# Kernel optimization log

Hardware: AMD Instinct MI355X
Metric: run time of the kernel (lower is better)

## Reference

```python
import jax, jax.numpy as jnp
import numpy as np

DIVISOR = 2.0
NEGATIVE_SLOPE = 0.01


def setup_inputs() -> dict:
    key = jax.random.key(0)
    k1, k2, k3 = jax.random.split(key, 3)
    x = jax.random.normal(k1, (32, 128, 130, 130), dtype=jnp.float32)
    weight = jax.random.normal(k2, (256, 128, 3, 3), dtype=jnp.float32) * 0.05
    bias = jax.random.normal(k3, (256,), dtype=jnp.float32)
    return {"x": x, "weight": weight, "bias": bias}


def reference(x, weight, bias):
    # conv2d, stride=1, padding=0 (VALID), NCHW / OIHW layout
    y = jax.lax.conv_general_dilated(
        x, weight,
        window_strides=(1, 1),
        padding='VALID',
        dimension_numbers=('NCHW', 'OIHW', 'NCHW'),
    )
    y = y + bias[None, :, None, None]
    y = y * (1.0 / DIVISOR)
    # fused LeakyReLU epilogue
    return jnp.where(y >= 0, y, y * NEGATIVE_SLOPE)
```

## Files before the change

kernel.cpp:

```cpp
#include <hip/hip_runtime.h>
#include <hip/hip_bf16.h>
#include <stdint.h>

typedef __bf16 bf16x8 __attribute__((ext_vector_type(8)));
typedef float  f32x4  __attribute__((ext_vector_type(4)));

#define NSLOPE 0.01f

#define NB   32
#define CIN  128
#define HIN  130
#define WIN  130
#define KOUT 256
#define POUT 128
#define QOUT 128
#define HWIN (HIN*WIN)
#define PQ   (POUT*QOUT)

#define XP_BYTES 138444800ull
#define WP_ELEMS (2*3*3*KOUT*64)

#define XT_OFF    16384
#define LDS_TOTAL (16384 + 16640)

__device__ __forceinline__ unsigned short f2bf(float f) {
    unsigned u = __builtin_bit_cast(unsigned, f);
    u += 0x7FFFu + ((u >> 16) & 1u);
    return (unsigned short)(u >> 16);
}

__device__ __forceinline__ void g2lds16(const void* g, void* l) {
    __builtin_amdgcn_global_load_lds(
        (const __attribute__((address_space(1))) void*)g,
        (__attribute__((address_space(3))) void*)l,
        16, 0, 0);
}

__global__ __launch_bounds__(256) void k_conv_xw(const float* __restrict__ X,
                                                 const float* __restrict__ W,
                                                 unsigned short* __restrict__ Xp,
                                                 unsigned short* __restrict__ Wp) {
    __shared__ unsigned int tile[64*131];
    const int tid = threadIdx.x;

    if (blockIdx.x >= NB*HIN) {
        int e = (blockIdx.x - NB*HIN)*256 + tid;
        if (e < WP_ELEMS) {
            int ci = e & 63;
            int k  = (e >> 6) & 255;
            int rsIdx = e >> 14;
            int cc = rsIdx / 9; int rem = rsIdx - cc*9; int r = rem / 3, s = rem - r*3;
            int c = cc*64 + ci;
            Wp[e] = f2bf(W[(size_t)k*1152 + (size_t)c*9 + r*3 + s]);
        }
        return;
    }

    const int b = blockIdx.x;
    const int n = b / 130, h = b - n*130;
    const size_t in0 = (size_t)n*(CIN*(size_t)HWIN) + (size_t)h*WIN;
    for (int fi = tid; fi < 64*130; fi += 256) {
        const int c2 = fi / 130, w = fi - c2*130;
        const float lo = X[in0 + (size_t)(2*c2  )*HWIN + w];
        const float hi = X[in0 + (size_t)(2*c2+1)*HWIN + w];
        tile[c2*131 + w] = (unsigned)f2bf(lo) | ((unsigned)f2bf(hi) << 16);
    }
    __syncthreads();
    unsigned int* outp = (unsigned int*)(Xp + (size_t)b*(WIN*CIN));
    for (int oi = tid; oi < 2080; oi += 256) {
        const int w = oi >> 4, j4 = (oi & 15) << 2;
        uint4 v;
        v.x = tile[(j4+0)*131 + w];
        v.y = tile[(j4+1)*131 + w];
        v.z = tile[(j4+2)*131 + w];
        v.w = tile[(j4+3)*131 + w];
        *(uint4*)(outp + w*64 + j4) = v;
    }
}

template<int PRIO>
__device__ __forceinline__ void conv_body(
    const unsigned short* __restrict__ Xp,
    const unsigned short* __restrict__ Wp,
    const float* __restrict__ bias,
    float* __restrict__ out,
    unsigned char* smem, int tid, int L)
{
    const int lane = tid & 63;
    const int wm   = tid >> 6;
    const int l15  = lane & 15;
    const int kg16 = (lane >> 4) << 4;

    const int kh = L & 1;
    const int np = L >> 1;
    const int p  = np & 127;
    const int n  = np >> 7;

    f32x4 acc[4][8];
    #pragma unroll
    for (int i = 0; i < 4; ++i)
        #pragma unroll
        for (int j = 0; j < 8; ++j)
            acc[i][j] = (f32x4){0.f, 0.f, 0.f, 0.f};

    #pragma unroll 1
    for (int t = 0; t < 18; ++t) {
        const int cc = t / 9;
        const int rem = t - cc*9;
        const int r  = rem / 3;
        const int s  = rem - r*3;

        __syncthreads();

        {
            const unsigned short* wbase = Wp + (size_t)t*(KOUT*64) + (size_t)(kh*128)*64;
            #pragma unroll
            for (int it = 0; it < 8; ++it) {
                const int g    = it*128 + tid;
                const int phys = g << 4;
                const int row  = phys >> 7;
                const int cib  = (phys & 127) ^ ((row & 7) << 4);
                g2lds16(wbase + (size_t)row*64 + (cib >> 1), smem + phys);
            }
        }
        if (s == 0) {
            const unsigned short* xbase =
                Xp + ((size_t)((n*HIN + (p + r))*WIN))*CIN + cc*64;
            #pragma unroll
            for (int it = 0; it < 9; ++it) {
                const int g = it*128 + tid;
                if (g < 1040) {
                    const int phys = g << 4;
                    const int w    = phys >> 7;
                    const int cib  = (phys & 127) ^ ((w & 7) << 4);
                    g2lds16(xbase + (size_t)w*CIN + (cib >> 1), smem + XT_OFF + phys);
                }
            }
        }

        __syncthreads();

        #pragma unroll
        for (int kq = 0; kq < 2; ++kq) {
            const int cib0 = kq*64 + kg16;
            bf16x8 A[4], B[8];
            #pragma unroll
            for (int mf = 0; mf < 4; ++mf) {
                const int row = wm*64 + mf*16 + l15;
                A[mf] = *(const bf16x8*)(smem + row*128 + (cib0 ^ ((row & 7) << 4)));
            }
            #pragma unroll
            for (int nf = 0; nf < 8; ++nf) {
                const int g = nf*16 + l15 + s;
                B[nf] = *(const bf16x8*)(smem + XT_OFF + g*128 + (cib0 ^ ((g & 7) << 4)));
            }
            __builtin_amdgcn_s_setprio(PRIO + 1);
            #pragma unroll
            for (int mf = 0; mf < 4; ++mf)
                #pragma unroll
                for (int nf = 0; nf < 8; ++nf)
                    acc[mf][nf] = __builtin_amdgcn_mfma_f32_16x16x32_bf16(
                        A[mf], B[nf], acc[mf][nf], 0, 0, 0);
            __builtin_amdgcn_s_setprio(PRIO);
        }
    }

    const int kg = lane >> 4;
    #pragma unroll
    for (int mf = 0; mf < 4; ++mf) {
        const int kb = kh*128 + wm*64 + mf*16 + kg*4;
        const float4 bv = *(const float4*)(bias + kb);
        const float bj[4] = {bv.x, bv.y, bv.z, bv.w};
        #pragma unroll
        for (int nf = 0; nf < 8; ++nf) {
            const int q = nf*16 + l15;
            const size_t base = (((size_t)n*KOUT + kb)*POUT + p)*QOUT + q;
            #pragma unroll
            for (int j = 0; j < 4; ++j) {
                float y = (acc[mf][nf][j] + bj[j]) * 0.5f;
                out[base + (size_t)j*PQ] = (y >= 0.f) ? y : y*NSLOPE;
            }
        }
    }
}

__global__ __launch_bounds__(128, 2) void k_conv_main(
    const unsigned short* __restrict__ Xp,
    const unsigned short* __restrict__ Wp,
    const float* __restrict__ bias,
    float* __restrict__ out)
{
    __shared__ __align__(16) unsigned char smem[LDS_TOTAL];

    const int L = ((blockIdx.x & 7) << 10) | (blockIdx.x >> 3);

    if (blockIdx.x & 1) {
        __builtin_amdgcn_s_setprio(1);
        conv_body<1>(Xp, Wp, bias, out, smem, threadIdx.x, L);
    } else {
        conv_body<0>(Xp, Wp, bias, out, smem, threadIdx.x, L);
    }
}

extern "C" void kernel_launch(void* const* d_in, const int* in_sizes, int n_in,
                              void* d_out, int out_size, void* d_ws, size_t ws_size,
                              hipStream_t stream) {
    const float* X = (const float*)d_in[0];
    const float* W = (const float*)d_in[1];
    const float* B = (const float*)d_in[2];
    float* out = (float*)d_out;
    unsigned short* Xp = (unsigned short*)d_ws;
    unsigned short* Wp = (unsigned short*)((char*)d_ws + XP_BYTES);

    k_conv_xw  <<<NB*HIN + (WP_ELEMS + 255)/256, 256, 0, stream>>>(X, W, Xp, Wp);
    k_conv_main<<<8192, 128, 0, stream>>>(Xp, Wp, B, out);
}
```

Baseline: 391.3 us.

## Double-buffer weight tiles in LDS and prefetch next tap during MFMA

Weight tiles are now double-buffered in LDS. The next tap's weight slice is issued with global_load_lds before the current tap's MFMAs run. Explicit vmcnt waits and raw s_barrier calls with sched_barrier fences replace the two __syncthreads per iteration. The input row tile stays single-buffered and is loaded at the start of each filter row. LDS use per block grows by 16KB, which could limit occupancy, and the hand-placed waitcnts depend on the order in which loads are issued.

```diff
diff --git a/kernel.cpp b/kernel.cpp
--- a/kernel.cpp
+++ b/kernel.cpp
@@ -20,8 +20,12 @@
 #define XP_BYTES 138444800ull
 #define WP_ELEMS (2*3*3*KOUT*64)
 
-#define XT_OFF    16384
-#define LDS_TOTAL (16384 + 16640)
+#define WS_BYTES  16384
+#define XT_OFF    32768
+#define LDS_TOTAL (32768 + 16640)
+
+#define SB0()  __builtin_amdgcn_sched_barrier(0)
+#define VMW(n) asm volatile("s_waitcnt vmcnt(" #n ")" ::: "memory")
 
 __device__ __forceinline__ unsigned short f2bf(float f) {
     unsigned u = __builtin_bit_cast(unsigned, f);
@@ -75,6 +79,34 @@
         v.z = tile[(j4+2)*131 + w];
         v.w = tile[(j4+3)*131 + w];
         *(uint4*)(outp + w*64 + j4) = v;
+    }
+}
+
+__device__ __forceinline__ void stage_w128(const unsigned short* __restrict__ Wp,
+                                           unsigned char* lds, int rsidx, int kh, int tid) {
+    const unsigned short* wbase = Wp + (size_t)rsidx*(KOUT*64) + (size_t)(kh*128)*64;
+    #pragma unroll
+    for (int it = 0; it < 8; ++it) {
+        const int g    = it*128 + tid;
+        const int phys = g << 4;
+        const int row  = phys >> 7;
+        const int cib  = (phys & 127) ^ ((row & 7) << 4);
+        g2lds16(wbase + (size_t)row*64 + (cib >> 1), lds + phys);
+    }
+}
+
+__device__ __forceinline__ void stage_x128(const unsigned short* __restrict__ Xp,
+                                           unsigned char* lds, int n, int h, int cc, int tid) {
+    const unsigned short* xbase = Xp + ((size_t)((n*HIN + h)*WIN))*CIN + cc*64;
+    #pragma unroll
+    for (int it = 0; it < 9; ++it) {
+        const int g = it*128 + tid;
+        if (g < 1040) {
+            const int phys = g << 4;
+            const int w    = phys >> 7;
+            const int cib  = (phys & 127) ^ ((w & 7) << 4);
+            g2lds16(xbase + (size_t)w*CIN + (cib >> 1), lds + phys);
+        }
     }
 }
 
@@ -96,6 +128,8 @@
     const int p  = np & 127;
     const int n  = np >> 7;
 
+    unsigned char* xt = smem + XT_OFF;
+
     f32x4 acc[4][8];
     #pragma unroll
     for (int i = 0; i < 4; ++i)
@@ -103,42 +137,27 @@
         for (int j = 0; j < 8; ++j)
             acc[i][j] = (f32x4){0.f, 0.f, 0.f, 0.f};
 
+    stage_x128(Xp, xt, n, p, 0, tid);
+    stage_w128(Wp, smem, 0, kh, tid);
+
     #pragma unroll 1
     for (int t = 0; t < 18; ++t) {
-        const int cc = t / 9;
+        const int cc  = t / 9;
         const int rem = t - cc*9;
-        const int r  = rem / 3;
-        const int s  = rem - r*3;
-
-        __syncthreads();
-
-        {
-            const unsigned short* wbase = Wp + (size_t)t*(KOUT*64) + (size_t)(kh*128)*64;
-            #pragma unroll
-            for (int it = 0; it < 8; ++it) {
-                const int g    = it*128 + tid;
-                const int phys = g << 4;
-                const int row  = phys >> 7;
-                const int cib  = (phys & 127) ^ ((row & 7) << 4);
-                g2lds16(wbase + (size_t)row*64 + (cib >> 1), smem + phys);
-            }
-        }
-        if (s == 0) {
-            const unsigned short* xbase =
-                Xp + ((size_t)((n*HIN + (p + r))*WIN))*CIN + cc*64;
-            #pragma unroll
-            for (int it = 0; it < 9; ++it) {
-                const int g = it*128 + tid;
-                if (g < 1040) {
-                    const int phys = g << 4;
-                    const int w    = phys >> 7;
-                    const int cib  = (phys & 127) ^ ((w & 7) << 4);
-                    g2lds16(xbase + (size_t)w*CIN + (cib >> 1), smem + XT_OFF + phys);
-                }
-            }
-        }
-
-        __syncthreads();
+        const int r   = rem / 3;
+        const int s   = rem - r*3;
+        unsigned char* wsR = smem + (t & 1)*WS_BYTES;
+
+        if (s == 0 && t > 0)
+            stage_x128(Xp, xt, n, p + r, cc, tid);
+        if (t < 17) {
+            stage_w128(Wp, smem + ((t + 1) & 1)*WS_BYTES, t + 1, kh, tid);
+            VMW(8);
+        } else {
+            VMW(0);
+        }
+        __builtin_amdgcn_s_barrier();
+        SB0();
 
         #pragma unroll
         for (int kq = 0; kq < 2; ++kq) {
@@ -147,12 +166,12 @@
             #pragma unroll
             for (int mf = 0; mf < 4; ++mf) {
                 const int row = wm*64 + mf*16 + l15;
-                A[mf] = *(const bf16x8*)(smem + row*128 + (cib0 ^ ((row & 7) << 4)));
+                A[mf] = *(const bf16x8*)(wsR + row*128 + (cib0 ^ ((row & 7) << 4)));
             }
             #pragma unroll
             for (int nf = 0; nf < 8; ++nf) {
                 const int g = nf*16 + l15 + s;
-                B[nf] = *(const bf16x8*)(smem + XT_OFF + g*128 + (cib0 ^ ((g & 7) << 4)));
+                B[nf] = *(const bf16x8*)(xt + g*128 + (cib0 ^ ((g & 7) << 4)));
             }
             __builtin_amdgcn_s_setprio(PRIO + 1);
             #pragma unroll
@@ -163,6 +182,9 @@
                         A[mf], B[nf], acc[mf][nf], 0, 0, 0);
             __builtin_amdgcn_s_setprio(PRIO);
         }
+
+        SB0();
+        __builtin_amdgcn_s_barrier();
     }
 
     const int kg = lane >> 4;
```

Result: slower. 476.7 us (+21.8%).

## Fuse input bf16 conversion and transpose into conv main kernel

Applied to the files above, without the earlier changes.

Drops the separate pre-pass that converted X to a channels-last bf16 workspace. The conv kernel now loads fp32 NCHW input directly, packs it to bf16 in registers and stores it swizzled into LDS. This removes the workspace write and read traffic and one kernel's worth of work. In exchange, each block re-reads fp32 data, which is twice as large, with synchronous loads instead of async global-to-LDS copies, and repeats the conversion.

```diff
diff --git a/kernel.cpp b/kernel.cpp
--- a/kernel.cpp
+++ b/kernel.cpp
@@ -17,7 +17,6 @@
 #define HWIN (HIN*WIN)
 #define PQ   (POUT*QOUT)
 
-#define XP_BYTES 138444800ull
 #define WP_ELEMS (2*3*3*KOUT*64)
 
 #define XT_OFF    16384
@@ -36,51 +35,21 @@
         16, 0, 0);
 }
 
-__global__ __launch_bounds__(256) void k_conv_xw(const float* __restrict__ X,
-                                                 const float* __restrict__ W,
-                                                 unsigned short* __restrict__ Xp,
-                                                 unsigned short* __restrict__ Wp) {
-    __shared__ unsigned int tile[64*131];
-    const int tid = threadIdx.x;
-
-    if (blockIdx.x >= NB*HIN) {
-        int e = (blockIdx.x - NB*HIN)*256 + tid;
-        if (e < WP_ELEMS) {
-            int ci = e & 63;
-            int k  = (e >> 6) & 255;
-            int rsIdx = e >> 14;
-            int cc = rsIdx / 9; int rem = rsIdx - cc*9; int r = rem / 3, s = rem - r*3;
-            int c = cc*64 + ci;
-            Wp[e] = f2bf(W[(size_t)k*1152 + (size_t)c*9 + r*3 + s]);
-        }
-        return;
-    }
-
-    const int b = blockIdx.x;
-    const int n = b / 130, h = b - n*130;
-    const size_t in0 = (size_t)n*(CIN*(size_t)HWIN) + (size_t)h*WIN;
-    for (int fi = tid; fi < 64*130; fi += 256) {
-        const int c2 = fi / 130, w = fi - c2*130;
-        const float lo = X[in0 + (size_t)(2*c2  )*HWIN + w];
-        const float hi = X[in0 + (size_t)(2*c2+1)*HWIN + w];
-        tile[c2*131 + w] = (unsigned)f2bf(lo) | ((unsigned)f2bf(hi) << 16);
-    }
-    __syncthreads();
-    unsigned int* outp = (unsigned int*)(Xp + (size_t)b*(WIN*CIN));
-    for (int oi = tid; oi < 2080; oi += 256) {
-        const int w = oi >> 4, j4 = (oi & 15) << 2;
-        uint4 v;
-        v.x = tile[(j4+0)*131 + w];
-        v.y = tile[(j4+1)*131 + w];
-        v.z = tile[(j4+2)*131 + w];
-        v.w = tile[(j4+3)*131 + w];
-        *(uint4*)(outp + w*64 + j4) = v;
-    }
+__global__ __launch_bounds__(256) void k_conv_w(const float* __restrict__ W,
+                                                unsigned short* __restrict__ Wp) {
+    int e = blockIdx.x*256 + threadIdx.x;
+    if (e >= WP_ELEMS) return;
+    int ci = e & 63;
+    int k  = (e >> 6) & 255;
+    int rsIdx = e >> 14;
+    int cc = rsIdx / 9; int rem = rsIdx - cc*9; int r = rem / 3, s = rem - r*3;
+    int c = cc*64 + ci;
+    Wp[e] = f2bf(W[(size_t)k*1152 + (size_t)c*9 + r*3 + s]);
 }
 
 template<int PRIO>
 __device__ __forceinline__ void conv_body(
-    const unsigned short* __restrict__ Xp,
+    const float* __restrict__ X,
     const unsigned short* __restrict__ Wp,
     const float* __restrict__ bias,
     float* __restrict__ out,
@@ -95,6 +64,8 @@
     const int np = L >> 1;
     const int p  = np & 127;
     const int n  = np >> 7;
+
+    unsigned char* xt = smem + XT_OFF;
 
     f32x4 acc[4][8];
     #pragma unroll
@@ -124,16 +95,27 @@
             }
         }
         if (s == 0) {
-            const unsigned short* xbase =
-                Xp + ((size_t)((n*HIN + (p + r))*WIN))*CIN + cc*64;
+            const size_t in0 = (size_t)n*(CIN*(size_t)HWIN) + (size_t)(p + r)*WIN;
             #pragma unroll
-            for (int it = 0; it < 9; ++it) {
-                const int g = it*128 + tid;
-                if (g < 1040) {
-                    const int phys = g << 4;
-                    const int w    = phys >> 7;
-                    const int cib  = (phys & 127) ^ ((w & 7) << 4);
-                    g2lds16(xbase + (size_t)w*CIN + (cib >> 1), smem + XT_OFF + phys);
+            for (int g8 = 0; g8 < 4; ++g8) {
+                const int ci8   = wm*4 + g8;
+                const int cbase = cc*64 + ci8*8;
+                const float* src0 = X + in0 + (size_t)cbase*HWIN;
+                #pragma unroll
+                for (int pass = 0; pass < 3; ++pass) {
+                    const int w = pass*64 + lane;
+                    if (w < 130) {
+                        unsigned up[4];
+                        #pragma unroll
+                        for (int jp = 0; jp < 4; ++jp) {
+                            const float lo = src0[(size_t)(2*jp  )*HWIN + w];
+                            const float hi = src0[(size_t)(2*jp+1)*HWIN + w];
+                            up[jp] = (unsigned)f2bf(lo) | ((unsigned)f2bf(hi) << 16);
+                        }
+                        const int byte = w*128 + ((ci8*16) ^ ((w & 7) << 4));
+                        uint4 v; v.x = up[0]; v.y = up[1]; v.z = up[2]; v.w = up[3];
+                        *(uint4*)(xt + byte) = v;
+                    }
                 }
             }
         }
@@ -152,7 +134,7 @@
             #pragma unroll
             for (int nf = 0; nf < 8; ++nf) {
                 const int g = nf*16 + l15 + s;
-                B[nf] = *(const bf16x8*)(smem + XT_OFF + g*128 + (cib0 ^ ((g & 7) << 4)));
+                B[nf] = *(const bf16x8*)(xt + g*128 + (cib0 ^ ((g & 7) << 4)));
             }
             __builtin_amdgcn_s_setprio(PRIO + 1);
             #pragma unroll
@@ -185,7 +167,7 @@
 }
 
 __global__ __launch_bounds__(128, 2) void k_conv_main(
-    const unsigned short* __restrict__ Xp,
+    const float* __restrict__ X,
     const unsigned short* __restrict__ Wp,
     const float* __restrict__ bias,
     float* __restrict__ out)
@@ -196,9 +178,9 @@
 
     if (blockIdx.x & 1) {
         __builtin_amdgcn_s_setprio(1);
-        conv_body<1>(Xp, Wp, bias, out, smem, threadIdx.x, L);
+        conv_body<1>(X, Wp, bias, out, smem, threadIdx.x, L);
     } else {
-        conv_body<0>(Xp, Wp, bias, out, smem, threadIdx.x, L);
+        conv_body<0>(X, Wp, bias, out, smem, threadIdx.x, L);
     }
 }
 
@@ -209,9 +191,8 @@
     const float* W = (const float*)d_in[1];
     const float* B = (const float*)d_in[2];
     float* out = (float*)d_out;
-    unsigned short* Xp = (unsigned short*)d_ws;
-    unsigned short* Wp = (unsigned short*)((char*)d_ws + XP_BYTES);
+    unsigned short* Wp = (unsigned short*)d_ws;
 
-    k_conv_xw  <<<NB*HIN + (WP_ELEMS + 255)/256, 256, 0, stream>>>(X, W, Xp, Wp);
-    k_conv_main<<<8192, 128, 0, stream>>>(Xp, Wp, B, out);
+    k_conv_w   <<<(WP_ELEMS + 255)/256, 256, 0, stream>>>(W, Wp);
+    k_conv_main<<<8192, 128, 0, stream>>>(X, Wp, B, out);
 }
```

Result: slower. 467.5 us (+19.5%).
